# Performance work log

Hardware: AMD Instinct MI355X
Metric: run time of the kernel (lower is better)

The kernel has to match this reference:

```python
import jax, jax.numpy as jnp
import numpy as np

B, L, D, H, E = 8, 256, 128, 6, 32

def setup_inputs() -> dict:
    key = jax.random.key(0)
    ks = jax.random.split(key, 9)
    s = 0.02
    return {
        "x": jax.random.normal(ks[0], (B, L, D), jnp.float32),
        "weight_adj": jax.random.uniform(ks[1], (B, H, L, L), jnp.float32),
        "e": jax.random.normal(ks[2], (B, L, L, E), jnp.float32),
        "W_w": jax.random.normal(ks[3], (D, D), jnp.float32) * s,
        "W_b": jax.random.normal(ks[4], (D,), jnp.float32) * s,
        "Wx_w": jax.random.normal(ks[5], (H, H + 2 * D + E), jnp.float32) * s,
        "Wx_b": jax.random.normal(ks[6], (H,), jnp.float32) * s,
        "Wxx_w": jax.random.normal(ks[7], (D, D), jnp.float32) * s,
        "Wxx_b": jax.random.normal(ks[8], (D,), jnp.float32) * s,
    }

def reference(x, weight_adj, e, W_w, W_b, Wx_w, Wx_b, Wxx_w, Wxx_b):
    d = x.shape[-1]
    h = weight_adj.shape[1]
    # mean over heads, then graph conv + linear + relu
    adj_avg = weight_adj.mean(axis=1)                      # [B,L,L]
    gcn = jax.nn.relu(jnp.einsum('bij,bjd->bid', adj_avg, x) @ W_w.T + W_b)  # [B,L,d]
    # Wx applied to cat([weight_adj_perm, node_i, node_j, e], -1), decomposed
    # column-wise so the huge [B,L,L,2d+H+E] concat is never materialized;
    # math is identical to Linear(cat(...)).
    Wa  = Wx_w[:, :h]                 # [H,H]
    Wn1 = Wx_w[:, h:h + d]            # [H,d]
    Wn2 = Wx_w[:, h + d:h + 2 * d]    # [H,d]
    We  = Wx_w[:, h + 2 * d:]         # [H,E]
    adj_term = jnp.einsum('bhij,kh->bijk', weight_adj, Wa)   # [B,L,L,H]
    n1 = gcn @ Wn1.T                                          # [B,L,H] (row node)
    n2 = gcn @ Wn2.T                                          # [B,L,H] (col node)
    e_term = jnp.einsum('bije,ke->bijk', e, We)               # [B,L,L,H]
    new_adj = adj_term + n1[:, :, None, :] + n2[:, None, :, :] + e_term + Wx_b
    new_adj = jnp.transpose(new_adj, (0, 3, 1, 2))            # [B,H,L,L]
    out = gcn @ Wxx_w.T + Wxx_b                               # [B,L,d]
    return out, new_adj
```

## Files before the change

kernel.cpp:

```cpp
#include <hip/hip_runtime.h>

#define Bn 8
#define Ln 256
#define Dn 128
#define Hn 6
#define En 32
#define WXROW (Hn + 2*Dn + En)
#define ROWS 4

__global__ __launch_bounds__(256) void k_avg(
    const float* __restrict__ wadj, float* __restrict__ avg)
{
    const int g = blockIdx.x * 256 + threadIdx.x;
    const int j4 = g & 63;
    const int i  = (g >> 6) & 255;
    const int b  = g >> 14;
    const float4* w4 = (const float4*)wadj;
    float4 s = {0.f, 0.f, 0.f, 0.f};
    #pragma unroll
    for (int h = 0; h < Hn; ++h) {
        const float4 v = w4[(((size_t)b * Hn + h) * Ln + i) * (Ln / 4) + j4];
        s.x += v.x; s.y += v.y; s.z += v.z; s.w += v.w;
    }
    const float inv_h = 1.0f / 6.0f;
    s.x *= inv_h; s.y *= inv_h; s.z *= inv_h; s.w *= inv_h;
    ((float4*)avg)[g] = s;
}

__global__ __launch_bounds__(512) void k_gcn2(
    const float* __restrict__ x, const float* __restrict__ avg,
    const float* __restrict__ W_w, const float* __restrict__ W_b,
    const float* __restrict__ Wx_w,
    const float* __restrict__ Wxx_w, const float* __restrict__ Wxx_b,
    float* __restrict__ out, float* __restrict__ n1_ws, float* __restrict__ n2_ws)
{
    __shared__ float adj[ROWS][Ln];
    __shared__ float part[16][ROWS][Dn];
    __shared__ float t_s[ROWS][Dn];
    __shared__ float g_s[ROWS][Dn];

    const int t  = threadIdx.x;
    const int b  = blockIdx.x >> 6;
    const int i0 = (blockIdx.x & 63) * ROWS;

    if (t < 256)
        ((float4*)&adj[0][0])[t] = ((const float4*)avg)[((size_t)b << 14) + (i0 << 6) + t];
    __syncthreads();

    {
        const int q  = t >> 5;
        const int d4 = t & 31;
        float4 acc[ROWS];
        #pragma unroll
        for (int r = 0; r < ROWS; ++r) acc[r] = {0.f, 0.f, 0.f, 0.f};
        const float4* xp4  = (const float4*)(x + (size_t)b * Ln * Dn) + d4;
        const float4* adj4 = (const float4*)&adj[0][0];
        #pragma unroll
        for (int jj4 = 0; jj4 < 4; ++jj4) {
            const int j = q * 16 + jj4 * 4;
            const float4 xv0 = xp4[(size_t)(j + 0) * 32];
            const float4 xv1 = xp4[(size_t)(j + 1) * 32];
            const float4 xv2 = xp4[(size_t)(j + 2) * 32];
            const float4 xv3 = xp4[(size_t)(j + 3) * 32];
            #pragma unroll
            for (int r = 0; r < ROWS; ++r) {
                const float4 a = adj4[r * 64 + (j >> 2)];
                float4 v = acc[r];
                v.x = fmaf(a.x, xv0.x, v.x); v.y = fmaf(a.x, xv0.y, v.y);
                v.z = fmaf(a.x, xv0.z, v.z); v.w = fmaf(a.x, xv0.w, v.w);
                v.x = fmaf(a.y, xv1.x, v.x); v.y = fmaf(a.y, xv1.y, v.y);
                v.z = fmaf(a.y, xv1.z, v.z); v.w = fmaf(a.y, xv1.w, v.w);
                v.x = fmaf(a.z, xv2.x, v.x); v.y = fmaf(a.z, xv2.y, v.y);
                v.z = fmaf(a.z, xv2.z, v.z); v.w = fmaf(a.z, xv2.w, v.w);
                v.x = fmaf(a.w, xv3.x, v.x); v.y = fmaf(a.w, xv3.y, v.y);
                v.z = fmaf(a.w, xv3.z, v.z); v.w = fmaf(a.w, xv3.w, v.w);
                acc[r] = v;
            }
        }
        #pragma unroll
        for (int r = 0; r < ROWS; ++r)
            ((float4*)&part[q][r][0])[d4] = acc[r];
    }
    __syncthreads();

    {
        const int rr = t >> 7, d = t & 127;
        float s = 0.f;
        #pragma unroll
        for (int q = 0; q < 16; ++q) s += part[q][rr][d];
        t_s[rr][d] = s;
    }
    __syncthreads();

    {
        const int s = t >> 7, d = t & 127, c0 = s * 32;
        const float4* wr = (const float4*)(W_w + (size_t)d * Dn + c0);
        float acc[ROWS] = {0.f, 0.f, 0.f, 0.f};
        #pragma unroll
        for (int c4 = 0; c4 < 8; ++c4) {
            const float4 w = wr[c4];
            #pragma unroll
            for (int r = 0; r < ROWS; ++r) {
                const float4 u = ((const float4*)&t_s[r][c0])[c4];
                float a = acc[r];
                a = fmaf(u.x, w.x, a); a = fmaf(u.y, w.y, a);
                a = fmaf(u.z, w.z, a); a = fmaf(u.w, w.w, a);
                acc[r] = a;
            }
        }
        #pragma unroll
        for (int r = 0; r < ROWS; ++r) part[s][r][d] = acc[r];
    }
    __syncthreads();

    {
        const int rr = t >> 7, d = t & 127;
        const float v = part[0][rr][d] + part[1][rr][d] + part[2][rr][d]
                      + part[3][rr][d] + W_b[d];
        g_s[rr][d] = fmaxf(v, 0.f);
    }
    __syncthreads();

    {
        const int s = t >> 7, d = t & 127, c0 = s * 32;
        const float4* wr = (const float4*)(Wxx_w + (size_t)d * Dn + c0);
        float acc[ROWS] = {0.f, 0.f, 0.f, 0.f};
        #pragma unroll
        for (int c4 = 0; c4 < 8; ++c4) {
            const float4 w = wr[c4];
            #pragma unroll
            for (int r = 0; r < ROWS; ++r) {
                const float4 u = ((const float4*)&g_s[r][c0])[c4];
                float a = acc[r];
                a = fmaf(u.x, w.x, a); a = fmaf(u.y, w.y, a);
                a = fmaf(u.z, w.z, a); a = fmaf(u.w, w.w, a);
                acc[r] = a;
            }
        }
        __syncthreads();
        #pragma unroll
        for (int r = 0; r < ROWS; ++r) part[s][r][t & 127] = acc[r];
    }
    __syncthreads();

    {
        const int rr = t >> 7, d = t & 127;
        const float v = part[0][rr][d] + part[1][rr][d] + part[2][rr][d]
                      + part[3][rr][d] + Wxx_b[d];
        out[((size_t)b * Ln + (i0 + rr)) * Dn + d] = v;
    }

    if (t < ROWS * 2 * Hn) {
        const int r  = t / (2 * Hn);
        const int kk = t % (2 * Hn);
        const int k  = (kk < Hn) ? kk : (kk - Hn);
        const bool isn2 = (kk >= Hn);
        const float* wrow = Wx_w + (size_t)k * WXROW + Hn + (isn2 ? Dn : 0);
        float acc = 0.f;
        #pragma unroll 8
        for (int c = 0; c < Dn; ++c)
            acc = fmaf(g_s[r][c], wrow[c], acc);
        const size_t idx = ((size_t)b * Hn + k) * Ln + (i0 + r);
        if (isn2) n2_ws[idx] = acc;
        else      n1_ws[idx] = acc;
    }
}

#define EPAD 33
__global__ __launch_bounds__(256) void k_adj(
    const float* __restrict__ wadj, const float* __restrict__ e,
    const float* __restrict__ Wx_w, const float* __restrict__ Wx_b,
    const float* __restrict__ n1_ws, const float* __restrict__ n2_ws,
    float* __restrict__ new_adj)
{
    __shared__ float e_lds[128 * EPAD];
    __shared__ float Wa_s[Hn][Hn];
    __shared__ float We_s[Hn][En];
    __shared__ float bias_n1[Hn];

    const int t = threadIdx.x;
    const int b = blockIdx.x >> 8;
    const int i = blockIdx.x & 255;

    if (t < Hn * Hn) {
        const int k = t / Hn, h = t % Hn;
        Wa_s[k][h] = Wx_w[(size_t)k * WXROW + h];
    }
    if (t >= 64 && t < 64 + Hn * En) {
        const int q = t - 64, k = q / En, c = q % En;
        We_s[k][c] = Wx_w[(size_t)k * WXROW + Hn + 2 * Dn + c];
    }
    if (t >= 32 && t < 32 + Hn) {
        const int k = t - 32;
        bias_n1[k] = Wx_b[k] + n1_ws[((size_t)b * Hn + k) * Ln + i];
    }

    const float4* ep4 = (const float4*)(e + (((size_t)b * Ln + i) * Ln) * En);
    const int s  = t >> 7;
    const int jl = t & 127;

    #pragma unroll
    for (int cH = 0; cH < 2; ++cH) {
        __syncthreads();
        #pragma unroll
        for (int p = 0; p < 4; ++p) {
            const int idx = t + p * 256;
            const float4 v = ep4[cH * 1024 + idx];
            const int j = idx >> 3;
            const int c = (idx & 7) * 4;
            float* dst = &e_lds[j * EPAD + c];
            dst[0] = v.x; dst[1] = v.y; dst[2] = v.z; dst[3] = v.w;
        }
        __syncthreads();

        const int j = cH * 128 + jl;

        float wv[Hn];
        #pragma unroll
        for (int h = 0; h < Hn; ++h)
            wv[h] = wadj[(((size_t)b * Hn + h) * Ln + i) * Ln + j];

        const float* ev = &e_lds[jl * EPAD];

        #pragma unroll
        for (int kq = 0; kq < 3; ++kq) {
            const int k = s * 3 + kq;
            float acc = bias_n1[k] + n2_ws[((size_t)b * Hn + k) * Ln + j];
            #pragma unroll
            for (int h = 0; h < Hn; ++h)
                acc = fmaf(wv[h], Wa_s[k][h], acc);
            #pragma unroll
            for (int c = 0; c < En; ++c)
                acc = fmaf(ev[c], We_s[k][c], acc);
            new_adj[(((size_t)b * Hn + k) * Ln + i) * Ln + j] = acc;
        }
    }
}

extern "C" void kernel_launch(void* const* d_in, const int* in_sizes, int n_in,
                              void* d_out, int out_size, void* d_ws, size_t ws_size,
                              hipStream_t stream) {
    const float* x      = (const float*)d_in[0];
    const float* wadj   = (const float*)d_in[1];
    const float* e      = (const float*)d_in[2];
    const float* W_w    = (const float*)d_in[3];
    const float* W_b    = (const float*)d_in[4];
    const float* Wx_w   = (const float*)d_in[5];
    const float* Wx_b   = (const float*)d_in[6];
    const float* Wxx_w  = (const float*)d_in[7];
    const float* Wxx_b  = (const float*)d_in[8];

    float* out      = (float*)d_out;
    float* new_adj  = out + (size_t)Bn * Ln * Dn;

    float* n1_ws = (float*)d_ws;
    float* n2_ws = n1_ws + (size_t)Bn * Hn * Ln;
    float* avg   = n2_ws + (size_t)Bn * Hn * Ln;

    k_avg<<<(Bn * Ln * Ln / 4) / 256, 256, 0, stream>>>(wadj, avg);
    k_gcn2<<<Bn * (Ln / ROWS), 512, 0, stream>>>(x, avg, W_w, W_b, Wx_w,
                                                 Wxx_w, Wxx_b, out, n1_ws, n2_ws);
    k_adj<<<Bn * Ln, 256, 0, stream>>>(wadj, e, Wx_w, Wx_b, n1_ws, n2_ws, new_adj);
}
```

Before: 150.0 us.

## Fuse head-averaging into GCN kernel and retile to two rows per block

Removes the separate head-mean kernel and its global avg buffer by computing the per-row mean of weight_adj inside the GCN kernel. The GCN kernel now processes 2 rows per block with 256 threads (1024 blocks instead of 512), and its reductions are restructured. This drops one launch plus a write and read of the averaged matrix, in exchange for less x reuse per block, since x is reloaded for every 2 rows instead of every 4.

```diff
diff --git a/kernel.cpp b/kernel.cpp
--- a/kernel.cpp
+++ b/kernel.cpp
@@ -6,151 +6,138 @@
 #define Hn 6
 #define En 32
 #define WXROW (Hn + 2*Dn + En)
-#define ROWS 4
-
-__global__ __launch_bounds__(256) void k_avg(
-    const float* __restrict__ wadj, float* __restrict__ avg)
-{
-    const int g = blockIdx.x * 256 + threadIdx.x;
-    const int j4 = g & 63;
-    const int i  = (g >> 6) & 255;
-    const int b  = g >> 14;
-    const float4* w4 = (const float4*)wadj;
-    float4 s = {0.f, 0.f, 0.f, 0.f};
-    #pragma unroll
-    for (int h = 0; h < Hn; ++h) {
-        const float4 v = w4[(((size_t)b * Hn + h) * Ln + i) * (Ln / 4) + j4];
-        s.x += v.x; s.y += v.y; s.z += v.z; s.w += v.w;
-    }
-    const float inv_h = 1.0f / 6.0f;
-    s.x *= inv_h; s.y *= inv_h; s.z *= inv_h; s.w *= inv_h;
-    ((float4*)avg)[g] = s;
-}
-
-__global__ __launch_bounds__(512) void k_gcn2(
-    const float* __restrict__ x, const float* __restrict__ avg,
+
+__global__ __launch_bounds__(256, 4) void k_gcn3(
+    const float* __restrict__ x, const float* __restrict__ wadj,
     const float* __restrict__ W_w, const float* __restrict__ W_b,
     const float* __restrict__ Wx_w,
     const float* __restrict__ Wxx_w, const float* __restrict__ Wxx_b,
     float* __restrict__ out, float* __restrict__ n1_ws, float* __restrict__ n2_ws)
 {
-    __shared__ float adj[ROWS][Ln];
-    __shared__ float part[16][ROWS][Dn];
-    __shared__ float t_s[ROWS][Dn];
-    __shared__ float g_s[ROWS][Dn];
+    __shared__ float adj_s[2][Ln];
+    __shared__ float part[8][2][Dn];
+    __shared__ float t_adj[2][Dn];
+    __shared__ float red[2][2][Dn];
+    __shared__ float g_s[2][Dn];
 
     const int t  = threadIdx.x;
-    const int b  = blockIdx.x >> 6;
-    const int i0 = (blockIdx.x & 63) * ROWS;
-
-    if (t < 256)
-        ((float4*)&adj[0][0])[t] = ((const float4*)avg)[((size_t)b << 14) + (i0 << 6) + t];
+    const int b  = blockIdx.x >> 7;
+    const int i0 = (blockIdx.x & 127) * 2;
+
+    if (t < 128) {
+        const int r = t >> 6, j4 = t & 63;
+        const float4* w4 = (const float4*)wadj;
+        float4 s = {0.f, 0.f, 0.f, 0.f};
+        #pragma unroll
+        for (int h = 0; h < Hn; ++h) {
+            const float4 v = w4[(((size_t)b * Hn + h) * Ln + i0 + r) * 64 + j4];
+            s.x += v.x; s.y += v.y; s.z += v.z; s.w += v.w;
+        }
+        const float inv_h = 1.0f / 6.0f;
+        s.x *= inv_h; s.y *= inv_h; s.z *= inv_h; s.w *= inv_h;
+        *(float4*)&adj_s[r][j4 * 4] = s;
+    }
     __syncthreads();
 
     {
         const int q  = t >> 5;
         const int d4 = t & 31;
-        float4 acc[ROWS];
-        #pragma unroll
-        for (int r = 0; r < ROWS; ++r) acc[r] = {0.f, 0.f, 0.f, 0.f};
-        const float4* xp4  = (const float4*)(x + (size_t)b * Ln * Dn) + d4;
-        const float4* adj4 = (const float4*)&adj[0][0];
-        #pragma unroll
-        for (int jj4 = 0; jj4 < 4; ++jj4) {
-            const int j = q * 16 + jj4 * 4;
+        float4 a0 = {0.f, 0.f, 0.f, 0.f};
+        float4 a1 = {0.f, 0.f, 0.f, 0.f};
+        const float4* xp4 = (const float4*)(x + (size_t)b * Ln * Dn) + d4;
+        const int j0 = q * 32;
+        #pragma unroll
+        for (int jj4 = 0; jj4 < 8; ++jj4) {
+            const int j = j0 + jj4 * 4;
             const float4 xv0 = xp4[(size_t)(j + 0) * 32];
             const float4 xv1 = xp4[(size_t)(j + 1) * 32];
             const float4 xv2 = xp4[(size_t)(j + 2) * 32];
             const float4 xv3 = xp4[(size_t)(j + 3) * 32];
-            #pragma unroll
-            for (int r = 0; r < ROWS; ++r) {
-                const float4 a = adj4[r * 64 + (j >> 2)];
-                float4 v = acc[r];
-                v.x = fmaf(a.x, xv0.x, v.x); v.y = fmaf(a.x, xv0.y, v.y);
-                v.z = fmaf(a.x, xv0.z, v.z); v.w = fmaf(a.x, xv0.w, v.w);
-                v.x = fmaf(a.y, xv1.x, v.x); v.y = fmaf(a.y, xv1.y, v.y);
-                v.z = fmaf(a.y, xv1.z, v.z); v.w = fmaf(a.y, xv1.w, v.w);
-                v.x = fmaf(a.z, xv2.x, v.x); v.y = fmaf(a.z, xv2.y, v.y);
-                v.z = fmaf(a.z, xv2.z, v.z); v.w = fmaf(a.z, xv2.w, v.w);
-                v.x = fmaf(a.w, xv3.x, v.x); v.y = fmaf(a.w, xv3.y, v.y);
-                v.z = fmaf(a.w, xv3.z, v.z); v.w = fmaf(a.w, xv3.w, v.w);
-                acc[r] = v;
-            }
-        }
-        #pragma unroll
-        for (int r = 0; r < ROWS; ++r)
-            ((float4*)&part[q][r][0])[d4] = acc[r];
-    }
-    __syncthreads();
-
-    {
-        const int rr = t >> 7, d = t & 127;
+            const float c00 = adj_s[0][j + 0], c10 = adj_s[1][j + 0];
+            const float c01 = adj_s[0][j + 1], c11 = adj_s[1][j + 1];
+            const float c02 = adj_s[0][j + 2], c12 = adj_s[1][j + 2];
+            const float c03 = adj_s[0][j + 3], c13 = adj_s[1][j + 3];
+            a0.x = fmaf(c00, xv0.x, a0.x); a0.y = fmaf(c00, xv0.y, a0.y);
+            a0.z = fmaf(c00, xv0.z, a0.z); a0.w = fmaf(c00, xv0.w, a0.w);
+            a1.x = fmaf(c10, xv0.x, a1.x); a1.y = fmaf(c10, xv0.y, a1.y);
+            a1.z = fmaf(c10, xv0.z, a1.z); a1.w = fmaf(c10, xv0.w, a1.w);
+            a0.x = fmaf(c01, xv1.x, a0.x); a0.y = fmaf(c01, xv1.y, a0.y);
+            a0.z = fmaf(c01, xv1.z, a0.z); a0.w = fmaf(c01, xv1.w, a0.w);
+            a1.x = fmaf(c11, xv1.x, a1.x); a1.y = fmaf(c11, xv1.y, a1.y);
+            a1.z = fmaf(c11, xv1.z, a1.z); a1.w = fmaf(c11, xv1.w, a1.w);
+            a0.x = fmaf(c02, xv2.x, a0.x); a0.y = fmaf(c02, xv2.y, a0.y);
+            a0.z = fmaf(c02, xv2.z, a0.z); a0.w = fmaf(c02, xv2.w, a0.w);
+            a1.x = fmaf(c12, xv2.x, a1.x); a1.y = fmaf(c12, xv2.y, a1.y);
+            a1.z = fmaf(c12, xv2.z, a1.z); a1.w = fmaf(c12, xv2.w, a1.w);
+            a0.x = fmaf(c03, xv3.x, a0.x); a0.y = fmaf(c03, xv3.y, a0.y);
+            a0.z = fmaf(c03, xv3.z, a0.z); a0.w = fmaf(c03, xv3.w, a0.w);
+            a1.x = fmaf(c13, xv3.x, a1.x); a1.y = fmaf(c13, xv3.y, a1.y);
+            a1.z = fmaf(c13, xv3.z, a1.z); a1.w = fmaf(c13, xv3.w, a1.w);
+        }
+        *(float4*)&part[q][0][d4 * 4] = a0;
+        *(float4*)&part[q][1][d4 * 4] = a1;
+    }
+    __syncthreads();
+
+    {
+        const int r = t >> 7, d = t & 127;
         float s = 0.f;
         #pragma unroll
-        for (int q = 0; q < 16; ++q) s += part[q][rr][d];
-        t_s[rr][d] = s;
-    }
-    __syncthreads();
-
-    {
-        const int s = t >> 7, d = t & 127, c0 = s * 32;
+        for (int q = 0; q < 8; ++q) s += part[q][r][d];
+        t_adj[r][d] = s;
+    }
+    __syncthreads();
+
+    {
+        const int s = t >> 7, d = t & 127, c0 = s * 64;
         const float4* wr = (const float4*)(W_w + (size_t)d * Dn + c0);
-        float acc[ROWS] = {0.f, 0.f, 0.f, 0.f};
-        #pragma unroll
-        for (int c4 = 0; c4 < 8; ++c4) {
-            const float4 w = wr[c4];
-            #pragma unroll
-            for (int r = 0; r < ROWS; ++r) {
-                const float4 u = ((const float4*)&t_s[r][c0])[c4];
-                float a = acc[r];
-                a = fmaf(u.x, w.x, a); a = fmaf(u.y, w.y, a);
-                a = fmaf(u.z, w.z, a); a = fmaf(u.w, w.w, a);
-                acc[r] = a;
-            }
-        }
-        #pragma unroll
-        for (int r = 0; r < ROWS; ++r) part[s][r][d] = acc[r];
-    }
-    __syncthreads();
-
-    {
-        const int rr = t >> 7, d = t & 127;
-        const float v = part[0][rr][d] + part[1][rr][d] + part[2][rr][d]
-                      + part[3][rr][d] + W_b[d];
-        g_s[rr][d] = fmaxf(v, 0.f);
-    }
-    __syncthreads();
-
-    {
-        const int s = t >> 7, d = t & 127, c0 = s * 32;
+        float p0 = 0.f, p1 = 0.f;
+        #pragma unroll
+        for (int c4 = 0; c4 < 16; ++c4) {
+            const float4 w  = wr[c4];
+            const float4 u0 = *(const float4*)&t_adj[0][c0 + c4 * 4];
+            const float4 u1 = *(const float4*)&t_adj[1][c0 + c4 * 4];
+            p0 = fmaf(u0.x, w.x, p0); p0 = fmaf(u0.y, w.y, p0);
+            p0 = fmaf(u0.z, w.z, p0); p0 = fmaf(u0.w, w.w, p0);
+            p1 = fmaf(u1.x, w.x, p1); p1 = fmaf(u1.y, w.y, p1);
+            p1 = fmaf(u1.z, w.z, p1); p1 = fmaf(u1.w, w.w, p1);
+        }
+        red[s][0][d] = p0;
+        red[s][1][d] = p1;
+    }
+    __syncthreads();
+    {
+        const int r = t >> 7, d = t & 127;
+        const float v = red[0][r][d] + red[1][r][d] + W_b[d];
+        g_s[r][d] = fmaxf(v, 0.f);
+    }
+    __syncthreads();
+
+    {
+        const int s = t >> 7, d = t & 127, c0 = s * 64;
         const float4* wr = (const float4*)(Wxx_w + (size_t)d * Dn + c0);
-        float acc[ROWS] = {0.f, 0.f, 0.f, 0.f};
-        #pragma unroll
-        for (int c4 = 0; c4 < 8; ++c4) {
-            const float4 w = wr[c4];
-            #pragma unroll
-            for (int r = 0; r < ROWS; ++r) {
-                const float4 u = ((const float4*)&g_s[r][c0])[c4];
-                float a = acc[r];
-                a = fmaf(u.x, w.x, a); a = fmaf(u.y, w.y, a);
-                a = fmaf(u.z, w.z, a); a = fmaf(u.w, w.w, a);
-                acc[r] = a;
-            }
-        }
-        __syncthreads();
-        #pragma unroll
-        for (int r = 0; r < ROWS; ++r) part[s][r][t & 127] = acc[r];
-    }
-    __syncthreads();
-
-    {
-        const int rr = t >> 7, d = t & 127;
-        const float v = part[0][rr][d] + part[1][rr][d] + part[2][rr][d]
-                      + part[3][rr][d] + Wxx_b[d];
-        out[((size_t)b * Ln + (i0 + rr)) * Dn + d] = v;
-    }
-
-    if (t < ROWS * 2 * Hn) {
+        float p0 = 0.f, p1 = 0.f;
+        #pragma unroll
+        for (int c4 = 0; c4 < 16; ++c4) {
+            const float4 w  = wr[c4];
+            const float4 u0 = *(const float4*)&g_s[0][c0 + c4 * 4];
+            const float4 u1 = *(const float4*)&g_s[1][c0 + c4 * 4];
+            p0 = fmaf(u0.x, w.x, p0); p0 = fmaf(u0.y, w.y, p0);
+            p0 = fmaf(u0.z, w.z, p0); p0 = fmaf(u0.w, w.w, p0);
+            p1 = fmaf(u1.x, w.x, p1); p1 = fmaf(u1.y, w.y, p1);
+            p1 = fmaf(u1.z, w.z, p1); p1 = fmaf(u1.w, w.w, p1);
+        }
+        red[s][0][d] = p0;
+        red[s][1][d] = p1;
+    }
+    __syncthreads();
+    {
+        const int r = t >> 7, d = t & 127;
+        const float v = red[0][r][d] + red[1][r][d] + Wxx_b[d];
+        out[((size_t)b * Ln + (i0 + r)) * Dn + d] = v;
+    }
+
+    if (t < 2 * 2 * Hn) {
         const int r  = t / (2 * Hn);
         const int kk = t % (2 * Hn);
         const int k  = (kk < Hn) ? kk : (kk - Hn);
@@ -255,10 +242,8 @@
 
     float* n1_ws = (float*)d_ws;
     float* n2_ws = n1_ws + (size_t)Bn * Hn * Ln;
-    float* avg   = n2_ws + (size_t)Bn * Hn * Ln;
-
-    k_avg<<<(Bn * Ln * Ln / 4) / 256, 256, 0, stream>>>(wadj, avg);
-    k_gcn2<<<Bn * (Ln / ROWS), 512, 0, stream>>>(x, avg, W_w, W_b, Wx_w,
-                                                 Wxx_w, Wxx_b, out, n1_ws, n2_ws);
+
+    k_gcn3<<<Bn * (Ln / 2), 256, 0, stream>>>(x, wadj, W_w, W_b, Wx_w,
+                                              Wxx_w, Wxx_b, out, n1_ws, n2_ws);
     k_adj<<<Bn * Ln, 256, 0, stream>>>(wadj, e, Wx_w, Wx_b, n1_ws, n2_ws, new_adj);
 }
```

Result: slower. 155.3 us (+3.5%).
